# Performance work log

Measured on AMD Instinct MI355X. Metric: run time of the kernel, lower is better.

## Reference

```python
import jax, jax.numpy as jnp
import numpy as np

HIDDEN = 128
N_NODES = 200000
N_VISITED = 1024


def setup_inputs() -> dict:
    key = jax.random.key(0)
    ks = jax.random.split(key, 7)
    X = jax.random.normal(ks[0], (N_NODES, HIDDEN), dtype=jnp.float32)
    x = jax.random.normal(ks[1], (HIDDEN,), dtype=jnp.float32)
    s = 1.0 / np.sqrt(HIDDEN)
    Wq = jax.random.uniform(ks[2], (3 * HIDDEN, HIDDEN), jnp.float32, -s, s)
    Wk = jax.random.uniform(ks[3], (HIDDEN, HIDDEN), jnp.float32, -s, s)
    Wv = jax.random.uniform(ks[4], (HIDDEN, HIDDEN), jnp.float32, -s, s)
    Wo = jax.random.uniform(ks[5], (HIDDEN, HIDDEN), jnp.float32, -s, s)
    nodes_visited = jax.random.randint(ks[6], (N_VISITED,), 0, N_NODES, dtype=jnp.int32)
    return {
        "X": X, "x": x, "Wq": Wq, "Wk": Wk, "Wv": Wv, "Wo": Wo,
        "nodes_visited": nodes_visited,
        "starting_node": 0, "previous_node": 1,
    }


def reference(X, x, Wq, Wk, Wv, Wo, nodes_visited, starting_node, previous_node):
    # X: [n_nodes, 128]; x: [128]
    n_nodes = X.shape[0]
    # features_concat = [x ; X[start] ; X[prev]]  -> [3*128]
    features_concat = jnp.concatenate([x, X[starting_node], X[previous_node]])
    q = features_concat @ Wq              # [128]
    k = X @ Wk                            # [n_nodes, 128]
    v = X @ Wv                            # [n_nodes, 128]
    u = (k @ q) / jnp.sqrt(jnp.float32(HIDDEN))   # [n_nodes]
    # additive mask: 1 everywhere, 0 at visited nodes (faithful to original)
    mask = jnp.ones((n_nodes,), dtype=X.dtype).at[nodes_visited].set(0.0)
    # final_layer == False branch
    u_ = jax.nn.softmax(u + mask)         # [n_nodes]
    h = u_ @ v                            # [128]
    out = h @ Wo                          # [128]
    return out
```

## Files before the change

### kernel.cpp

```cpp
#include <hip/hip_runtime.h>
#include <math.h>

#define HIDDEN 128
#define MAIN_BLOCKS 512
#define MAIN_THREADS 1024
#define MAX_BMAP_WORDS 6272
#define FLAG_MAGIC 0x13579BDFu
#define FLAG_PAIR ((((unsigned long long)(~FLAG_MAGIC)) << 32) | (unsigned long long)FLAG_MAGIC)

__global__ __launch_bounds__(MAIN_THREADS, 8) void fused_all(
    const float* __restrict__ X, const float* __restrict__ x,
    const float* __restrict__ Wq, const float* __restrict__ Wk,
    const float* __restrict__ Wv, const float* __restrict__ Wo,
    const int* __restrict__ visited, int nv,
    const int* __restrict__ startp, const int* __restrict__ prevp,
    float* __restrict__ Mb, float* __restrict__ Sb, float* __restrict__ Gb,
    unsigned long long* __restrict__ flag64,
    float* __restrict__ out, int n)
{
    __shared__ unsigned bmap[MAX_BMAP_WORDS];
    __shared__ float fc[384];
    __shared__ float qpart[8][HIDDEN];
    __shared__ float qv[HIDDEN];
    __shared__ float qks[HIDDEN];
    __shared__ float m_arr[32];
    __shared__ float s_arr[32];
    __shared__ float g_all[32 * HIDDEN];
    __shared__ float fin_red[MAIN_THREADS];
    __shared__ float fin_e[MAIN_BLOCKS];

    const int tid  = threadIdx.x;
    const int lane = tid & 63;
    const int sub  = lane & 31;
    const int half = (lane >> 5) & 1;

    const int nwords = (n + 31) >> 5;
    float fcv = 0.f;
    if (tid < 384) {
        if (tid < 128)      fcv = x[tid];
        else if (tid < 256) fcv = X[(size_t)startp[0] * HIDDEN + (tid - 128)];
        else                fcv = X[(size_t)prevp[0]  * HIDDEN + (tid - 256)];
    }
    for (int w = tid; w < nwords; w += MAIN_THREADS) bmap[w] = 0u;
    if (tid < 384) fc[tid] = fcv;
    __syncthreads();

    for (int i = tid; i < nv; i += MAIN_THREADS) {
        const int v = visited[i];
        atomicOr(&bmap[v >> 5], 1u << (v & 31));
    }
    {
        const int col = tid & (HIDDEN - 1);
        const int seg = tid >> 7;
        const int m0  = seg * 48;
        float acc = 0.f;
        #pragma unroll 8
        for (int m = 0; m < 48; ++m)
            acc += fc[m0 + m] * Wq[(size_t)(m0 + m) * HIDDEN + col];
        qpart[seg][col] = acc;
    }
    __syncthreads();
    if (tid < HIDDEN)
        qv[tid] = ((qpart[0][tid] + qpart[1][tid]) + (qpart[2][tid] + qpart[3][tid]))
                + ((qpart[4][tid] + qpart[5][tid]) + (qpart[6][tid] + qpart[7][tid]));
    __syncthreads();

    {
        const int hw0 = tid >> 5;
        const float4 qv4 = *(const float4*)(&qv[sub << 2]);
        #pragma unroll
        for (int k = 0; k < 4; ++k) {
            const int row = hw0 + (k << 5);
            const float4 wk4 = *(const float4*)(Wk + (size_t)row * HIDDEN + (sub << 2));
            float p = wk4.x * qv4.x + wk4.y * qv4.y + wk4.z * qv4.z + wk4.w * qv4.w;
            #pragma unroll
            for (int off = 16; off >= 1; off >>= 1)
                p += __shfl_xor(p, off, 64);
            if (sub == 0) qks[row] = p * 0.08838834764831845f;
        }
    }
    __syncthreads();

    const int wavesPerBlock = MAIN_THREADS >> 6;
    const int gw    = blockIdx.x * wavesPerBlock + (tid >> 6);
    const int rstep = gridDim.x * wavesPerBlock * 8;

    const float4 qkv = *(const float4*)(&qks[sub << 2]);
    const float4 Z   = make_float4(0.f, 0.f, 0.f, 0.f);

    float m = -INFINITY, s = 0.f;
    float g0 = 0.f, g1 = 0.f, g2 = 0.f, g3 = 0.f;

    for (int rb = gw * 8 + half * 4; rb < n; rb += rstep) {
        const int r0 = rb, r1 = rb + 1, r2 = rb + 2, r3 = rb + 3;
        const float4 xv0 = *(const float4*)(X + (size_t)r0 * HIDDEN + (sub << 2));
        const float4 xv1 = (r1 < n) ? *(const float4*)(X + (size_t)r1 * HIDDEN + (sub << 2)) : Z;
        const float4 xv2 = (r2 < n) ? *(const float4*)(X + (size_t)r2 * HIDDEN + (sub << 2)) : Z;
        const float4 xv3 = (r3 < n) ? *(const float4*)(X + (size_t)r3 * HIDDEN + (sub << 2)) : Z;

        float p0 = xv0.x * qkv.x + xv0.y * qkv.y + xv0.z * qkv.z + xv0.w * qkv.w;
        float p1 = xv1.x * qkv.x + xv1.y * qkv.y + xv1.z * qkv.z + xv1.w * qkv.w;
        float p2 = xv2.x * qkv.x + xv2.y * qkv.y + xv2.z * qkv.z + xv2.w * qkv.w;
        float p3 = xv3.x * qkv.x + xv3.y * qkv.y + xv3.z * qkv.z + xv3.w * qkv.w;
        #pragma unroll
        for (int off = 16; off >= 1; off >>= 1) {
            p0 += __shfl_xor(p0, off, 64);
            p1 += __shfl_xor(p1, off, 64);
            p2 += __shfl_xor(p2, off, 64);
            p3 += __shfl_xor(p3, off, 64);
        }
        const float u0 =            p0 + (((bmap[r0 >> 5] >> (r0 & 31)) & 1u) ? 0.f : 1.f);
        const float u1 = (r1 < n) ? p1 + (((bmap[r1 >> 5] >> (r1 & 31)) & 1u) ? 0.f : 1.f) : -INFINITY;
        const float u2 = (r2 < n) ? p2 + (((bmap[r2 >> 5] >> (r2 & 31)) & 1u) ? 0.f : 1.f) : -INFINITY;
        const float u3 = (r3 < n) ? p3 + (((bmap[r3 >> 5] >> (r3 & 31)) & 1u) ? 0.f : 1.f) : -INFINITY;

        const float umax = fmaxf(fmaxf(u0, u1), fmaxf(u2, u3));
        const float mn = fmaxf(m, umax);
        const float sc = __expf(m - mn);
        const float w0 = __expf(u0 - mn);
        const float w1 = __expf(u1 - mn);
        const float w2 = __expf(u2 - mn);
        const float w3 = __expf(u3 - mn);
        s  = s  * sc + ((w0 + w1) + (w2 + w3));
        g0 = g0 * sc + (w0 * xv0.x + w1 * xv1.x) + (w2 * xv2.x + w3 * xv3.x);
        g1 = g1 * sc + (w0 * xv0.y + w1 * xv1.y) + (w2 * xv2.y + w3 * xv3.y);
        g2 = g2 * sc + (w0 * xv0.z + w1 * xv1.z) + (w2 * xv2.z + w3 * xv3.z);
        g3 = g3 * sc + (w0 * xv0.w + w1 * xv1.w) + (w2 * xv2.w + w3 * xv3.w);
        m  = mn;
    }

    const int hw = tid >> 5;
    *(float4*)(&g_all[hw * HIDDEN + (sub << 2)]) = make_float4(g0, g1, g2, g3);
    if (sub == 0) { m_arr[hw] = m; s_arr[hw] = s; }
    __syncthreads();

    float mb = m_arr[0];
    #pragma unroll
    for (int h = 1; h < 32; ++h) mb = fmaxf(mb, m_arr[h]);

    if (tid < HIDDEN) {
        float G = 0.f;
        #pragma unroll 4
        for (int h = 0; h < 32; ++h)
            G += g_all[h * HIDDEN + tid] * __expf(m_arr[h] - mb);
        __hip_atomic_store(&Gb[blockIdx.x * HIDDEN + tid], G,
                           __ATOMIC_RELAXED, __HIP_MEMORY_SCOPE_AGENT);
    } else if (tid == HIDDEN) {
        float S = 0.f;
        #pragma unroll
        for (int h = 0; h < 32; ++h) S += s_arr[h] * __expf(m_arr[h] - mb);
        __hip_atomic_store(&Sb[blockIdx.x], S,
                           __ATOMIC_RELAXED, __HIP_MEMORY_SCOPE_AGENT);
        __hip_atomic_store(&Mb[blockIdx.x], mb,
                           __ATOMIC_RELAXED, __HIP_MEMORY_SCOPE_AGENT);
    }

    __syncthreads();
    if (tid == 0) {
        __hip_atomic_store(&flag64[blockIdx.x], FLAG_PAIR,
                           __ATOMIC_RELAXED, __HIP_MEMORY_SCOPE_AGENT);
    }

    if (blockIdx.x != MAIN_BLOCKS - 1) return;

    if (tid < 64) {
        #pragma unroll
        for (int k = 0; k < MAIN_BLOCKS / 64; ++k) {
            const int b = tid + (k << 6);
            while (__hip_atomic_load(&flag64[b], __ATOMIC_RELAXED,
                                     __HIP_MEMORY_SCOPE_AGENT) != FLAG_PAIR) {
                __builtin_amdgcn_s_sleep(2);
            }
        }
    }
    __syncthreads();

    const float mt = (tid < MAIN_BLOCKS)
        ? __hip_atomic_load(&Mb[tid], __ATOMIC_RELAXED, __HIP_MEMORY_SCOPE_AGENT)
        : -INFINITY;
    fin_red[tid] = mt; __syncthreads();
    for (int st = 512; st >= 1; st >>= 1) {
        if (tid < st) fin_red[tid] = fmaxf(fin_red[tid], fin_red[tid + st]);
        __syncthreads();
    }
    const float M = fin_red[0];
    __syncthreads();

    float ls = 0.f;
    if (tid < MAIN_BLOCKS) {
        const float eb = __expf(mt - M);
        fin_e[tid] = eb;
        ls = __hip_atomic_load(&Sb[tid], __ATOMIC_RELAXED,
                               __HIP_MEMORY_SCOPE_AGENT) * eb;
    }
    fin_red[tid] = ls; __syncthreads();
    for (int st = 512; st >= 1; st >>= 1) {
        if (tid < st) fin_red[tid] += fin_red[tid + st];
        __syncthreads();
    }
    const float S = fin_red[0];
    __syncthreads();

    const int col = tid & (HIDDEN - 1);
    const int seg = tid >> 7;

    {
        const int b0 = seg * (MAIN_BLOCKS / 8);
        float acc = 0.f;
        #pragma unroll 8
        for (int b = 0; b < MAIN_BLOCKS / 8; ++b)
            acc += __hip_atomic_load(&Gb[(size_t)(b0 + b) * HIDDEN + col],
                                     __ATOMIC_RELAXED, __HIP_MEMORY_SCOPE_AGENT)
                   * fin_e[b0 + b];
        qpart[seg][col] = acc;
    }
    __syncthreads();
    if (tid < HIDDEN)
        qv[tid] = (((qpart[0][tid] + qpart[1][tid]) + (qpart[2][tid] + qpart[3][tid]))
                 + ((qpart[4][tid] + qpart[5][tid]) + (qpart[6][tid] + qpart[7][tid]))) / S;
    __syncthreads();

    {
        const int m0 = seg * 16;
        float acc = 0.f;
        #pragma unroll
        for (int m2 = 0; m2 < 16; ++m2)
            acc += qv[m0 + m2] * Wv[(size_t)(m0 + m2) * HIDDEN + col];
        qpart[seg][col] = acc;
    }
    __syncthreads();
    if (tid < HIDDEN)
        qks[tid] = ((qpart[0][tid] + qpart[1][tid]) + (qpart[2][tid] + qpart[3][tid]))
                 + ((qpart[4][tid] + qpart[5][tid]) + (qpart[6][tid] + qpart[7][tid]));
    __syncthreads();

    {
        const int m0 = seg * 16;
        float acc = 0.f;
        #pragma unroll
        for (int m2 = 0; m2 < 16; ++m2)
            acc += qks[m0 + m2] * Wo[(size_t)(m0 + m2) * HIDDEN + col];
        qpart[seg][col] = acc;
    }
    __syncthreads();
    if (tid < HIDDEN)
        out[tid] = ((qpart[0][tid] + qpart[1][tid]) + (qpart[2][tid] + qpart[3][tid]))
                 + ((qpart[4][tid] + qpart[5][tid]) + (qpart[6][tid] + qpart[7][tid]));
}

extern "C" void kernel_launch(void* const* d_in, const int* in_sizes, int n_in,
                              void* d_out, int out_size, void* d_ws, size_t ws_size,
                              hipStream_t stream)
{
    const float* X       = (const float*)d_in[0];
    const float* x       = (const float*)d_in[1];
    const float* Wq      = (const float*)d_in[2];
    const float* Wk      = (const float*)d_in[3];
    const float* Wv      = (const float*)d_in[4];
    const float* Wo      = (const float*)d_in[5];
    const int*   visited = (const int*)d_in[6];
    const int*   startp  = (const int*)d_in[7];
    const int*   prevp   = (const int*)d_in[8];

    const int n  = in_sizes[0] / HIDDEN;
    const int nv = in_sizes[6];

    float* ws = (float*)d_ws;
    float* Mb = ws + 128;
    float* Sb = Mb + MAIN_BLOCKS;
    float* Gb = Sb + MAIN_BLOCKS;
    unsigned long long* flag64 =
        (unsigned long long*)(Gb + (size_t)MAIN_BLOCKS * HIDDEN);

    fused_all<<<MAIN_BLOCKS, MAIN_THREADS, 0, stream>>>(
        X, x, Wq, Wk, Wv, Wo, visited, nv, startp, prevp,
        Mb, Sb, Gb, flag64, (float*)d_out, n);
}
```

Measured before the change: 181.7 us.

## Split fused kernel into stream and finish kernels, drop flag spin-wait

Replaces the last-block spin-wait on per-block flags with a second single-block launch that does the final softmax merge and the Wv/Wo projections. Plain stores and loads replace the atomic ones, and the flag array is removed. This avoids the cost of the spin-polling block and the flag traffic, but adds a second kernel launch and the gap between the two kernels.

Measured after the change: 182.1 us. No clear change (+0.2%).

```diff
diff --git a/kernel.cpp b/kernel.cpp
--- a/kernel.cpp
+++ b/kernel.cpp
@@ -5,18 +5,14 @@
 #define MAIN_BLOCKS 512
 #define MAIN_THREADS 1024
 #define MAX_BMAP_WORDS 6272
-#define FLAG_MAGIC 0x13579BDFu
-#define FLAG_PAIR ((((unsigned long long)(~FLAG_MAGIC)) << 32) | (unsigned long long)FLAG_MAGIC)
-
-__global__ __launch_bounds__(MAIN_THREADS, 8) void fused_all(
+
+__global__ __launch_bounds__(MAIN_THREADS, 8) void stream_kernel(
     const float* __restrict__ X, const float* __restrict__ x,
     const float* __restrict__ Wq, const float* __restrict__ Wk,
-    const float* __restrict__ Wv, const float* __restrict__ Wo,
     const int* __restrict__ visited, int nv,
     const int* __restrict__ startp, const int* __restrict__ prevp,
     float* __restrict__ Mb, float* __restrict__ Sb, float* __restrict__ Gb,
-    unsigned long long* __restrict__ flag64,
-    float* __restrict__ out, int n)
+    int n)
 {
     __shared__ unsigned bmap[MAX_BMAP_WORDS];
     __shared__ float fc[384];
@@ -26,8 +22,6 @@
     __shared__ float m_arr[32];
     __shared__ float s_arr[32];
     __shared__ float g_all[32 * HIDDEN];
-    __shared__ float fin_red[MAIN_THREADS];
-    __shared__ float fin_e[MAIN_BLOCKS];
 
     const int tid  = threadIdx.x;
     const int lane = tid & 63;
@@ -143,81 +137,65 @@
         #pragma unroll 4
         for (int h = 0; h < 32; ++h)
             G += g_all[h * HIDDEN + tid] * __expf(m_arr[h] - mb);
-        __hip_atomic_store(&Gb[blockIdx.x * HIDDEN + tid], G,
-                           __ATOMIC_RELAXED, __HIP_MEMORY_SCOPE_AGENT);
+        Gb[blockIdx.x * HIDDEN + tid] = G;
     } else if (tid == HIDDEN) {
         float S = 0.f;
         #pragma unroll
         for (int h = 0; h < 32; ++h) S += s_arr[h] * __expf(m_arr[h] - mb);
-        __hip_atomic_store(&Sb[blockIdx.x], S,
-                           __ATOMIC_RELAXED, __HIP_MEMORY_SCOPE_AGENT);
-        __hip_atomic_store(&Mb[blockIdx.x], mb,
-                           __ATOMIC_RELAXED, __HIP_MEMORY_SCOPE_AGENT);
-    }
-
-    __syncthreads();
-    if (tid == 0) {
-        __hip_atomic_store(&flag64[blockIdx.x], FLAG_PAIR,
-                           __ATOMIC_RELAXED, __HIP_MEMORY_SCOPE_AGENT);
-    }
-
-    if (blockIdx.x != MAIN_BLOCKS - 1) return;
-
-    if (tid < 64) {
-        #pragma unroll
-        for (int k = 0; k < MAIN_BLOCKS / 64; ++k) {
-            const int b = tid + (k << 6);
-            while (__hip_atomic_load(&flag64[b], __ATOMIC_RELAXED,
-                                     __HIP_MEMORY_SCOPE_AGENT) != FLAG_PAIR) {
-                __builtin_amdgcn_s_sleep(2);
-            }
-        }
-    }
-    __syncthreads();
-
-    const float mt = (tid < MAIN_BLOCKS)
-        ? __hip_atomic_load(&Mb[tid], __ATOMIC_RELAXED, __HIP_MEMORY_SCOPE_AGENT)
-        : -INFINITY;
-    fin_red[tid] = mt; __syncthreads();
+        Sb[blockIdx.x] = S;
+        Mb[blockIdx.x] = mb;
+    }
+}
+
+__global__ __launch_bounds__(MAIN_THREADS) void finish_kernel(
+    const float* __restrict__ Mb, const float* __restrict__ Sb,
+    const float* __restrict__ Gb,
+    const float* __restrict__ Wv, const float* __restrict__ Wo,
+    float* __restrict__ out)
+{
+    __shared__ float red[MAIN_THREADS];
+    __shared__ float e[MAIN_BLOCKS];
+    __shared__ float part[8][HIDDEN];
+    __shared__ float pvec[HIDDEN];
+    __shared__ float hvec[HIDDEN];
+
+    const int tid = threadIdx.x;
+    const int col = tid & (HIDDEN - 1);
+    const int seg = tid >> 7;
+
+    const float mt = (tid < MAIN_BLOCKS) ? Mb[tid] : -INFINITY;
+    red[tid] = mt; __syncthreads();
     for (int st = 512; st >= 1; st >>= 1) {
-        if (tid < st) fin_red[tid] = fmaxf(fin_red[tid], fin_red[tid + st]);
+        if (tid < st) red[tid] = fmaxf(red[tid], red[tid + st]);
         __syncthreads();
     }
-    const float M = fin_red[0];
+    const float M = red[0];
     __syncthreads();
 
     float ls = 0.f;
     if (tid < MAIN_BLOCKS) {
-        const float eb = __expf(mt - M);
-        fin_e[tid] = eb;
-        ls = __hip_atomic_load(&Sb[tid], __ATOMIC_RELAXED,
-                               __HIP_MEMORY_SCOPE_AGENT) * eb;
-    }
-    fin_red[tid] = ls; __syncthreads();
+        const float eb = __expf(mt - M); e[tid] = eb; ls = Sb[tid] * eb;
+    }
+    red[tid] = ls; __syncthreads();
     for (int st = 512; st >= 1; st >>= 1) {
-        if (tid < st) fin_red[tid] += fin_red[tid + st];
+        if (tid < st) red[tid] += red[tid + st];
         __syncthreads();
     }
-    const float S = fin_red[0];
-    __syncthreads();
-
-    const int col = tid & (HIDDEN - 1);
-    const int seg = tid >> 7;
+    const float S = red[0];
+    __syncthreads();
 
     {
         const int b0 = seg * (MAIN_BLOCKS / 8);
         float acc = 0.f;
         #pragma unroll 8
         for (int b = 0; b < MAIN_BLOCKS / 8; ++b)
-            acc += __hip_atomic_load(&Gb[(size_t)(b0 + b) * HIDDEN + col],
-                                     __ATOMIC_RELAXED, __HIP_MEMORY_SCOPE_AGENT)
-                   * fin_e[b0 + b];
-        qpart[seg][col] = acc;
-    }
-    __syncthreads();
-    if (tid < HIDDEN)
-        qv[tid] = (((qpart[0][tid] + qpart[1][tid]) + (qpart[2][tid] + qpart[3][tid]))
-                 + ((qpart[4][tid] + qpart[5][tid]) + (qpart[6][tid] + qpart[7][tid]))) / S;
+            acc += Gb[(size_t)(b0 + b) * HIDDEN + col] * e[b0 + b];
+        part[seg][col] = acc;
+    }
+    __syncthreads();
+    if (tid < HIDDEN)
+        pvec[tid] = (((part[0][tid] + part[1][tid]) + (part[2][tid] + part[3][tid]))
+                   + ((part[4][tid] + part[5][tid]) + (part[6][tid] + part[7][tid]))) / S;
     __syncthreads();
 
     {
@@ -225,13 +203,13 @@
         float acc = 0.f;
         #pragma unroll
         for (int m2 = 0; m2 < 16; ++m2)
-            acc += qv[m0 + m2] * Wv[(size_t)(m0 + m2) * HIDDEN + col];
-        qpart[seg][col] = acc;
-    }
-    __syncthreads();
-    if (tid < HIDDEN)
-        qks[tid] = ((qpart[0][tid] + qpart[1][tid]) + (qpart[2][tid] + qpart[3][tid]))
-                 + ((qpart[4][tid] + qpart[5][tid]) + (qpart[6][tid] + qpart[7][tid]));
+            acc += pvec[m0 + m2] * Wv[(size_t)(m0 + m2) * HIDDEN + col];
+        part[seg][col] = acc;
+    }
+    __syncthreads();
+    if (tid < HIDDEN)
+        hvec[tid] = ((part[0][tid] + part[1][tid]) + (part[2][tid] + part[3][tid]))
+                  + ((part[4][tid] + part[5][tid]) + (part[6][tid] + part[7][tid]));
     __syncthreads();
 
     {
@@ -239,13 +217,13 @@
         float acc = 0.f;
         #pragma unroll
         for (int m2 = 0; m2 < 16; ++m2)
-            acc += qks[m0 + m2] * Wo[(size_t)(m0 + m2) * HIDDEN + col];
-        qpart[seg][col] = acc;
-    }
-    __syncthreads();
-    if (tid < HIDDEN)
-        out[tid] = ((qpart[0][tid] + qpart[1][tid]) + (qpart[2][tid] + qpart[3][tid]))
-                 + ((qpart[4][tid] + qpart[5][tid]) + (qpart[6][tid] + qpart[7][tid]));
+            acc += hvec[m0 + m2] * Wo[(size_t)(m0 + m2) * HIDDEN + col];
+        part[seg][col] = acc;
+    }
+    __syncthreads();
+    if (tid < HIDDEN)
+        out[tid] = ((part[0][tid] + part[1][tid]) + (part[2][tid] + part[3][tid]))
+                 + ((part[4][tid] + part[5][tid]) + (part[6][tid] + part[7][tid]));
 }
 
 extern "C" void kernel_launch(void* const* d_in, const int* in_sizes, int n_in,
@@ -269,10 +247,9 @@
     float* Mb = ws + 128;
     float* Sb = Mb + MAIN_BLOCKS;
     float* Gb = Sb + MAIN_BLOCKS;
-    unsigned long long* flag64 =
-        (unsigned long long*)(Gb + (size_t)MAIN_BLOCKS * HIDDEN);
-
-    fused_all<<<MAIN_BLOCKS, MAIN_THREADS, 0, stream>>>(
-        X, x, Wq, Wk, Wv, Wo, visited, nv, startp, prevp,
-        Mb, Sb, Gb, flag64, (float*)d_out, n);
+
+    stream_kernel<<<MAIN_BLOCKS, MAIN_THREADS, 0, stream>>>(
+        X, x, Wq, Wk, visited, nv, startp, prevp, Mb, Sb, Gb, n);
+    finish_kernel<<<1, MAIN_THREADS, 0, stream>>>(
+        Mb, Sb, Gb, Wv, Wo, (float*)d_out);
 }
```
